# Optimization experiments

Measured on AMD Instinct MI355X. Metric: run time of the kernel, lower is better.

Reference implementation:

```python
import jax, jax.numpy as jnp
import numpy as np
from jax import lax

RADIUS = 8
EPS = 0.01


def box_filter(x, r):
    # Sum over a (2r+1)x(2r+1) window with zero ('same') padding — identical math
    # to depthwise conv2d with a ones kernel and padding=r.
    k = 2 * r + 1
    return lax.reduce_window(
        x, jnp.array(0, x.dtype), lax.add,
        window_dimensions=(1, 1, k, k),
        window_strides=(1, 1, 1, 1),
        padding=((0, 0), (0, 0), (r, r), (r, r)),
    )


def setup_inputs() -> dict:
    key = jax.random.key(0)
    k1, k2 = jax.random.split(key)
    shape = (16, 3, 512, 512)
    I = jax.random.uniform(k1, shape, dtype=jnp.float32)
    p = jax.random.uniform(k2, shape, dtype=jnp.float32)
    return {"I": I, "p": p}


def reference(I, p):
    r = RADIUS
    eps = EPS
    N = box_filter(jnp.ones_like(I), r)          # window pixel counts (handles borders)
    mean_I = box_filter(I, r) / N
    mean_p = box_filter(p, r) / N
    mean_Ip = box_filter(I * p, r) / N
    cov_Ip = mean_Ip - mean_I * mean_p
    mean_II = box_filter(I * I, r) / N
    var_I = mean_II - mean_I * mean_I
    a = cov_Ip / (var_I + eps)
    b = mean_p - a * mean_I
    mean_a = box_filter(a, r) / N
    mean_b = box_filter(b, r) / N
    q = mean_a * I + mean_b
    return q
```

## Files before the change

kernel.cpp:

```cpp
#include <hip/hip_runtime.h>


#define RAD  8
#define H    512
#define W    512
#define TILE 32
#define KCH  4
#define EPS  0.01f

__global__ __launch_bounds__(512, 4)
void guided_filter_kernel(const float* __restrict__ Ig,
                          const float* __restrict__ Pg,
                          float* __restrict__ out)
{
    __shared__ __align__(16) float4 F4[64 * 32];
    __shared__ __align__(16) float4 H4[64 * 48];

    float2* F2p = (float2*)F4;
    float2* AB  = (float2*)F4;
    float2* HAB = (float2*)F4 + 48 * 50;

    const int tid   = threadIdx.x;
    const int plane = blockIdx.z;
    const int x0 = blockIdx.x * TILE - 2 * RAD;
    const int Y0 = blockIdx.y * (TILE * KCH);
    const float* Ib = Ig + (size_t)plane * (H * W);
    const float* Pb = Pg + (size_t)plane * (H * W);
    float* Ob = out + (size_t)plane * (H * W);

    auto stage_raw64 = [&](int ybase) {
        const bool interior = (x0 >= 0) && (ybase >= 0) &&
                              (x0 + 64 <= W) && (ybase + 64 <= H);
        if (interior) {
            #pragma unroll
            for (int it = 0; it < 2; ++it) {
                int idx = it * 512 + tid;
                int ry = idx >> 4, f4 = idx & 15;
                int rl = ry & 7, pf = ry & 1;
                const float* ip = Ib + (ybase + ry) * W + x0 + 4 * f4;
                const float* pp = Pb + (ybase + ry) * W + x0 + 4 * f4;
                float4 iv = *(const float4*)ip;
                float4 pv = *(const float4*)pp;
                float2 e0 = make_float2(iv.x, pv.x), e1 = make_float2(iv.y, pv.y);
                float2 e2 = make_float2(iv.z, pv.z), e3 = make_float2(iv.w, pv.w);
                float2 a0 = pf ? e1 : e0, a1 = pf ? e0 : e1;
                float2 b0 = pf ? e3 : e2, b1 = pf ? e2 : e3;
                float4* Fr = &F4[ry * 32];
                Fr[(2 * f4) ^ rl]     = make_float4(a0.x, a0.y, a1.x, a1.y);
                Fr[(2 * f4 + 1) ^ rl] = make_float4(b0.x, b0.y, b1.x, b1.y);
            }
        } else {
            #pragma unroll
            for (int it = 0; it < 2; ++it) {
                int idx = it * 512 + tid;
                int ry = idx >> 4, f4 = idx & 15;
                int rl = ry & 7, pf = ry & 1;
                int gy = ybase + ry;
                float2 el[4];
                #pragma unroll
                for (int k = 0; k < 4; ++k) {
                    int gx = x0 + 4 * f4 + k;
                    bool v = ((unsigned)gy < (unsigned)H) && ((unsigned)gx < (unsigned)W);
                    el[k].x = v ? Ib[gy * W + gx] : 0.f;
                    el[k].y = v ? Pb[gy * W + gx] : 0.f;
                }
                float2 a0 = pf ? el[1] : el[0], a1 = pf ? el[0] : el[1];
                float2 b0 = pf ? el[3] : el[2], b1 = pf ? el[2] : el[3];
                float4* Fr = &F4[ry * 32];
                Fr[(2 * f4) ^ rl]     = make_float4(a0.x, a0.y, a1.x, a1.y);
                Fr[(2 * f4 + 1) ^ rl] = make_float4(b0.x, b0.y, b1.x, b1.y);
            }
        }
    };

    auto stage_load = [&](int ybase, float4& iv, float4& pv) {
        const int ry = tid >> 4, f4 = tid & 15;
        const int gy = ybase + ry;
        const bool interior = (x0 >= 0) && (x0 + 64 <= W) &&
                              (ybase >= 0) && (ybase + 32 <= H);
        if (interior) {
            iv = *(const float4*)(Ib + gy * W + x0 + 4 * f4);
            pv = *(const float4*)(Pb + gy * W + x0 + 4 * f4);
        } else {
            float* fi = (float*)&iv;
            float* fp = (float*)&pv;
            #pragma unroll
            for (int k = 0; k < 4; ++k) {
                int gx = x0 + 4 * f4 + k;
                bool v = ((unsigned)gy < (unsigned)H) && ((unsigned)gx < (unsigned)W);
                fi[k] = v ? Ib[gy * W + gx] : 0.f;
                fp[k] = v ? Pb[gy * W + gx] : 0.f;
            }
        }
    };
    auto stage_write = [&](float4 iv, float4 pv) {
        const int ry = tid >> 4, f4 = tid & 15;
        const int rl = ry & 7, pf = ry & 1;
        float2 e0 = make_float2(iv.x, pv.x), e1 = make_float2(iv.y, pv.y);
        float2 e2 = make_float2(iv.z, pv.z), e3 = make_float2(iv.w, pv.w);
        float2 a0 = pf ? e1 : e0, a1 = pf ? e0 : e1;
        float2 b0 = pf ? e3 : e2, b1 = pf ? e2 : e3;
        float4* Fr = &F4[ry * 32];
        Fr[(2 * f4) ^ rl]     = make_float4(a0.x, a0.y, a1.x, a1.y);
        Fr[(2 * f4 + 1) ^ rl] = make_float4(b0.x, b0.y, b1.x, b1.y);
    };

    auto s2_rows = [&](int tbase, bool full) {
        if (full || tid < 256) {
            const int r  = tid >> 3, e = tid & 7;
            const int rl = r & 7, pf = r & 1;
            const int c0 = 6 * e;
            const float4* Fr = &F4[r * 32];
            const float2* Er = &F2p[r * 64];
            float4 S = make_float4(0.f, 0.f, 0.f, 0.f);
            const int gb = 3 * e;
            #pragma unroll
            for (int m = 0; m < 8; ++m) {
                float4 fr = Fr[(gb + m) ^ rl];
                S.x += fr.x + fr.z;
                S.y += fr.y + fr.w;
                S.z += fr.x * fr.y + fr.z * fr.w;
                S.w += fr.x * fr.x + fr.z * fr.z;
            }
            {
                int c = c0 + 16;
                float2 v = Er[(((c >> 1) ^ rl) << 1) | pf];
                S.x += v.x; S.y += v.y; S.z += v.x * v.y; S.w += v.x * v.x;
            }
            const int slot = (tbase + r) & 63;
            float4* Hrow = &H4[slot * 48];
            #pragma unroll
            for (int k = 0; k < 6; ++k) {
                Hrow[(c0 + k) ^ rl] = S;
                if (k < 5) {
                    int ca = c0 + k + 17, cs = c0 + k;
                    float2 va = Er[(((ca >> 1) ^ rl) << 1) | ((ca & 1) ^ pf)];
                    float2 vs = Er[(((cs >> 1) ^ rl) << 1) | ((cs & 1) ^ pf)];
                    S.x += va.x - vs.x;
                    S.y += va.y - vs.y;
                    S.z += va.x * va.y - vs.x * vs.y;
                    S.w += va.x * va.x - vs.x * vs.x;
                }
            }
        }
    };

    auto s3g = [&](int g) {
        if (tid < 384) {
            const int col = tid % 48, chunk = tid / 48;
            const int cy0 = chunk * 6;
            const int tb = 32 * g;
            float4 S = make_float4(0.f, 0.f, 0.f, 0.f);
            #pragma unroll
            for (int j = 0; j < 17; ++j) {
                int row = tb + cy0 + j;
                float4 v = H4[(row & 63) * 48 + (col ^ (row & 7))];
                S.x += v.x; S.y += v.y; S.z += v.z; S.w += v.w;
            }
            int gx = x0 + RAD + col;
            int nx = min(gx + RAD, W - 1) - max(gx - RAD, 0) + 1;
            #pragma unroll
            for (int k = 0; k < 6; ++k) {
                int cy = cy0 + k;
                int gy = Y0 + 32 * g - RAD + cy;
                float a = 0.f, b = 0.f;
                if (((unsigned)gy < (unsigned)H) && ((unsigned)gx < (unsigned)W)) {
                    int ny = min(gy + RAD, H - 1) - max(gy - RAD, 0) + 1;
                    float invN = __builtin_amdgcn_rcpf((float)(nx * ny));
                    float mI = S.x * invN, mp = S.y * invN;
                    float cov = S.z * invN - mI * mp;
                    float var = S.w * invN - mI * mI;
                    a = cov * __builtin_amdgcn_rcpf(var + EPS);
                    b = mp - a * mI;
                }
                AB[cy * 50 + col] = make_float2(a, b);
                if (k < 5) {
                    int ra = tb + cy + 17, rs = tb + cy;
                    float4 va = H4[(ra & 63) * 48 + (col ^ (ra & 7))];
                    float4 vs = H4[(rs & 63) * 48 + (col ^ (rs & 7))];
                    S.x += va.x - vs.x; S.y += va.y - vs.y;
                    S.z += va.z - vs.z; S.w += va.w - vs.w;
                }
            }
        }
    };

    auto s4 = [&]() {
        if (tid < 384) {
            const int r = tid % 48, e = tid / 48;
            const int c0 = 4 * e;
            const float2* row  = &AB[r * 50];
            const float4* rowg = (const float4*)row;
            float2 S = make_float2(0.f, 0.f);
            #pragma unroll
            for (int m = 0; m < 8; ++m) {
                float4 gq = rowg[2 * e + m];
                S.x += gq.x + gq.z;
                S.y += gq.y + gq.w;
            }
            {
                float2 v = row[c0 + 16];
                S.x += v.x; S.y += v.y;
            }
            #pragma unroll
            for (int k = 0; k < 4; ++k) {
                HAB[r * 33 + c0 + k] = S;
                if (k < 3) {
                    float2 va = row[c0 + k + 17];
                    float2 vs = row[c0 + k];
                    S.x += va.x - vs.x; S.y += va.y - vs.y;
                }
            }
        }
    };

    auto s5g = [&](int g) {
        const int col = tid & 31, chunk = tid >> 5;
        const int oy0 = chunk * 2;
        float2 S = make_float2(0.f, 0.f);
        #pragma unroll
        for (int j = 0; j < 17; ++j) {
            float2 v = HAB[(oy0 + j) * 33 + col];
            S.x += v.x; S.y += v.y;
        }
        int gx = x0 + 2 * RAD + col;
        int nx = min(gx + RAD, W - 1) - max(gx - RAD, 0) + 1;
        #pragma unroll
        for (int k = 0; k < 2; ++k) {
            int oy = oy0 + k;
            int gy = Y0 + 32 * g + oy;
            int ny = min(gy + RAD, H - 1) - max(gy - RAD, 0) + 1;
            float invN = __builtin_amdgcn_rcpf((float)(nx * ny));
            float iv = Ib[gy * W + gx];
            Ob[gy * W + gx] = S.x * invN * iv + S.y * invN;
            if (k < 1) {
                float2 va = HAB[(oy + 17) * 33 + col];
                float2 vs = HAB[oy * 33 + col];
                S.x += va.x - vs.x; S.y += va.y - vs.y;
            }
        }
    };

    stage_raw64(Y0 - 2 * RAD);
    __syncthreads();
    s2_rows(0, true);
    float4 siv, spv;
    #pragma unroll 1
    for (int g = 0; g < KCH; ++g) {
        if (g < KCH - 1)
            stage_load(Y0 + 32 * g + 48, siv, spv);
        __syncthreads();
        s3g(g);
        __syncthreads();
        s4();
        __syncthreads();
        if (g < KCH - 1)
            stage_write(siv, spv);
        s5g(g);
        if (g < KCH - 1) {
            __syncthreads();
            s2_rows(32 * g + 64, false);
        }
    }
}

extern "C" void kernel_launch(void* const* d_in, const int* in_sizes, int n_in,
                              void* d_out, int out_size, void* d_ws, size_t ws_size,
                              hipStream_t stream) {
    const float* I = (const float*)d_in[0];
    const float* P = (const float*)d_in[1];
    float* out = (float*)d_out;
    int planes = in_sizes[0] / (H * W);
    dim3 grid(W / TILE, H / (TILE * KCH), planes);
    guided_filter_kernel<<<grid, dim3(512), 0, stream>>>(I, P, out);
}
```

Baseline: 262.1 us.

## Warp-specialize tail: half the block stages next rows while other half writes outputs

```diff
diff --git a/kernel.cpp b/kernel.cpp
--- a/kernel.cpp
+++ b/kernel.cpp
@@ -27,6 +27,43 @@
     const float* Ib = Ig + (size_t)plane * (H * W);
     const float* Pb = Pg + (size_t)plane * (H * W);
     float* Ob = out + (size_t)plane * (H * W);
+
+    auto s2_row = [&](int r, int e, int tbase) {
+        const int rl = r & 7, pf = r & 1;
+        const int c0 = 6 * e;
+        const float4* Fr = &F4[r * 32];
+        const float2* Er = &F2p[r * 64];
+        float4 S = make_float4(0.f, 0.f, 0.f, 0.f);
+        const int gb = 3 * e;
+        #pragma unroll
+        for (int m = 0; m < 8; ++m) {
+            float4 fr = Fr[(gb + m) ^ rl];
+            S.x += fr.x + fr.z;
+            S.y += fr.y + fr.w;
+            S.z += fr.x * fr.y + fr.z * fr.w;
+            S.w += fr.x * fr.x + fr.z * fr.z;
+        }
+        {
+            int c = c0 + 16;
+            float2 v = Er[(((c >> 1) ^ rl) << 1) | pf];
+            S.x += v.x; S.y += v.y; S.z += v.x * v.y; S.w += v.x * v.x;
+        }
+        const int slot = (tbase + r) & 63;
+        float4* Hrow = &H4[slot * 48];
+        #pragma unroll
+        for (int k = 0; k < 6; ++k) {
+            Hrow[(c0 + k) ^ rl] = S;
+            if (k < 5) {
+                int ca = c0 + k + 17, cs = c0 + k;
+                float2 va = Er[(((ca >> 1) ^ rl) << 1) | ((ca & 1) ^ pf)];
+                float2 vs = Er[(((cs >> 1) ^ rl) << 1) | ((cs & 1) ^ pf)];
+                S.x += va.x - vs.x;
+                S.y += va.y - vs.y;
+                S.z += va.x * va.y - vs.x * vs.y;
+                S.w += va.x * va.x - vs.x * vs.x;
+            }
+        }
+    };
 
     auto stage_raw64 = [&](int ybase) {
         const bool interior = (x0 >= 0) && (ybase >= 0) &&
@@ -73,76 +110,40 @@
         }
     };
 
-    auto stage_load = [&](int ybase, float4& iv, float4& pv) {
-        const int ry = tid >> 4, f4 = tid & 15;
+    auto tail_stage_s2 = [&](int g) {
+        const int ry = tid >> 3, sub = tid & 7;
+        const int ybase = Y0 + 32 * g + 48;
+        const int rl = ry & 7, pf = ry & 1;
         const int gy = ybase + ry;
         const bool interior = (x0 >= 0) && (x0 + 64 <= W) &&
                               (ybase >= 0) && (ybase + 32 <= H);
-        if (interior) {
-            iv = *(const float4*)(Ib + gy * W + x0 + 4 * f4);
-            pv = *(const float4*)(Pb + gy * W + x0 + 4 * f4);
-        } else {
-            float* fi = (float*)&iv;
-            float* fp = (float*)&pv;
-            #pragma unroll
-            for (int k = 0; k < 4; ++k) {
-                int gx = x0 + 4 * f4 + k;
-                bool v = ((unsigned)gy < (unsigned)H) && ((unsigned)gx < (unsigned)W);
-                fi[k] = v ? Ib[gy * W + gx] : 0.f;
-                fp[k] = v ? Pb[gy * W + gx] : 0.f;
-            }
-        }
-    };
-    auto stage_write = [&](float4 iv, float4 pv) {
-        const int ry = tid >> 4, f4 = tid & 15;
-        const int rl = ry & 7, pf = ry & 1;
-        float2 e0 = make_float2(iv.x, pv.x), e1 = make_float2(iv.y, pv.y);
-        float2 e2 = make_float2(iv.z, pv.z), e3 = make_float2(iv.w, pv.w);
-        float2 a0 = pf ? e1 : e0, a1 = pf ? e0 : e1;
-        float2 b0 = pf ? e3 : e2, b1 = pf ? e2 : e3;
         float4* Fr = &F4[ry * 32];
-        Fr[(2 * f4) ^ rl]     = make_float4(a0.x, a0.y, a1.x, a1.y);
-        Fr[(2 * f4 + 1) ^ rl] = make_float4(b0.x, b0.y, b1.x, b1.y);
-    };
-
-    auto s2_rows = [&](int tbase, bool full) {
-        if (full || tid < 256) {
-            const int r  = tid >> 3, e = tid & 7;
-            const int rl = r & 7, pf = r & 1;
-            const int c0 = 6 * e;
-            const float4* Fr = &F4[r * 32];
-            const float2* Er = &F2p[r * 64];
-            float4 S = make_float4(0.f, 0.f, 0.f, 0.f);
-            const int gb = 3 * e;
-            #pragma unroll
-            for (int m = 0; m < 8; ++m) {
-                float4 fr = Fr[(gb + m) ^ rl];
-                S.x += fr.x + fr.z;
-                S.y += fr.y + fr.w;
-                S.z += fr.x * fr.y + fr.z * fr.w;
-                S.w += fr.x * fr.x + fr.z * fr.z;
-            }
-            {
-                int c = c0 + 16;
-                float2 v = Er[(((c >> 1) ^ rl) << 1) | pf];
-                S.x += v.x; S.y += v.y; S.z += v.x * v.y; S.w += v.x * v.x;
-            }
-            const int slot = (tbase + r) & 63;
-            float4* Hrow = &H4[slot * 48];
-            #pragma unroll
-            for (int k = 0; k < 6; ++k) {
-                Hrow[(c0 + k) ^ rl] = S;
-                if (k < 5) {
-                    int ca = c0 + k + 17, cs = c0 + k;
-                    float2 va = Er[(((ca >> 1) ^ rl) << 1) | ((ca & 1) ^ pf)];
-                    float2 vs = Er[(((cs >> 1) ^ rl) << 1) | ((cs & 1) ^ pf)];
-                    S.x += va.x - vs.x;
-                    S.y += va.y - vs.y;
-                    S.z += va.x * va.y - vs.x * vs.y;
-                    S.w += va.x * va.x - vs.x * vs.x;
-                }
-            }
-        }
+        #pragma unroll
+        for (int h = 0; h < 2; ++h) {
+            const int f4 = 2 * sub + h;
+            float4 iv, pv;
+            if (interior) {
+                iv = *(const float4*)(Ib + gy * W + x0 + 4 * f4);
+                pv = *(const float4*)(Pb + gy * W + x0 + 4 * f4);
+            } else {
+                float* fi = (float*)&iv;
+                float* fp = (float*)&pv;
+                #pragma unroll
+                for (int k = 0; k < 4; ++k) {
+                    int gx = x0 + 4 * f4 + k;
+                    bool v = ((unsigned)gy < (unsigned)H) && ((unsigned)gx < (unsigned)W);
+                    fi[k] = v ? Ib[gy * W + gx] : 0.f;
+                    fp[k] = v ? Pb[gy * W + gx] : 0.f;
+                }
+            }
+            float2 e0 = make_float2(iv.x, pv.x), e1 = make_float2(iv.y, pv.y);
+            float2 e2 = make_float2(iv.z, pv.z), e3 = make_float2(iv.w, pv.w);
+            float2 a0 = pf ? e1 : e0, a1 = pf ? e0 : e1;
+            float2 b0 = pf ? e3 : e2, b1 = pf ? e2 : e3;
+            Fr[(2 * f4) ^ rl]     = make_float4(a0.x, a0.y, a1.x, a1.y);
+            Fr[(2 * f4 + 1) ^ rl] = make_float4(b0.x, b0.y, b1.x, b1.y);
+        }
+        s2_row(ry, sub, 32 * g + 64);
     };
 
     auto s3g = [&](int g) {
@@ -215,8 +216,9 @@
     };
 
     auto s5g = [&](int g) {
-        const int col = tid & 31, chunk = tid >> 5;
-        const int oy0 = chunk * 2;
+        const int t2 = tid - 256;
+        const int col = t2 & 31, chunk = t2 >> 5;
+        const int oy0 = chunk * 4;
         float2 S = make_float2(0.f, 0.f);
         #pragma unroll
         for (int j = 0; j < 17; ++j) {
@@ -226,14 +228,14 @@
         int gx = x0 + 2 * RAD + col;
         int nx = min(gx + RAD, W - 1) - max(gx - RAD, 0) + 1;
         #pragma unroll
-        for (int k = 0; k < 2; ++k) {
+        for (int k = 0; k < 4; ++k) {
             int oy = oy0 + k;
             int gy = Y0 + 32 * g + oy;
             int ny = min(gy + RAD, H - 1) - max(gy - RAD, 0) + 1;
             float invN = __builtin_amdgcn_rcpf((float)(nx * ny));
             float iv = Ib[gy * W + gx];
             Ob[gy * W + gx] = S.x * invN * iv + S.y * invN;
-            if (k < 1) {
+            if (k < 3) {
                 float2 va = HAB[(oy + 17) * 33 + col];
                 float2 vs = HAB[oy * 33 + col];
                 S.x += va.x - vs.x; S.y += va.y - vs.y;
@@ -243,23 +245,18 @@
 
     stage_raw64(Y0 - 2 * RAD);
     __syncthreads();
-    s2_rows(0, true);
-    float4 siv, spv;
+    s2_row(tid >> 3, tid & 7, 0);
     #pragma unroll 1
     for (int g = 0; g < KCH; ++g) {
-        if (g < KCH - 1)
-            stage_load(Y0 + 32 * g + 48, siv, spv);
         __syncthreads();
         s3g(g);
         __syncthreads();
         s4();
         __syncthreads();
-        if (g < KCH - 1)
-            stage_write(siv, spv);
-        s5g(g);
-        if (g < KCH - 1) {
-            __syncthreads();
-            s2_rows(32 * g + 64, false);
+        if (tid < 256) {
+            if (g < KCH - 1) tail_stage_s2(g);
+        } else {
+            s5g(g);
         }
     }
 }
```

Measured after the change: 262.7 us. No clear change (+0.2%).
